# Kernel tuning notes

Measured on AMD Instinct MI355X. Metric: run time of the kernel, lower is better.

The kernel has to match this reference:

```python
import jax, jax.numpy as jnp
import numpy as np

NUM_LOW, NUM_HIGH, DIM = 8192, 1024, 2048
EPS = 1e-10


def sparsemax(z):
    # z: [..., K]; Martins & Astudillo sparsemax along last axis.
    K = z.shape[-1]
    z_sorted = jnp.flip(jnp.sort(z, axis=-1), axis=-1)          # descending
    z_cum = jnp.cumsum(z_sorted, axis=-1)
    k = jnp.arange(1, K + 1, dtype=z.dtype)
    support = (1.0 + k * z_sorted) > z_cum                       # bool [..., K]
    k_sup = jnp.sum(support, axis=-1, keepdims=True)             # int [..., 1]
    tau = (jnp.take_along_axis(z_cum, k_sup - 1, axis=-1) - 1.0) / k_sup.astype(z.dtype)
    return jnp.maximum(z - tau, 0.0)


def normalize_rows(x, eps=EPS):
    return x / (jnp.sum(x, axis=1, keepdims=True) + eps)


def setup_inputs() -> dict:
    key = jax.random.key(0)
    k1, k2, k3, k4 = jax.random.split(key, 4)

    def xavier(k, shape):
        bound = float(np.sqrt(6.0 / (shape[0] + shape[1])))
        return jax.random.uniform(k, shape, jnp.float32, -bound, bound)

    return {
        "low_w": xavier(k1, (NUM_LOW, DIM)),    # low Concepts parameter
        "high_w": xavier(k2, (NUM_HIGH, DIM)),  # high Concepts parameter
        "Wq": xavier(k3, (DIM, DIM)),           # q_linear.weight (keep_head_dim, n_head=1)
        "Wk": xavier(k4, (DIM, DIM)),           # k_linear.weight
        "norm_low_concepts": 1,
        "norm_high_concepts": 1,
    }


def reference(low_w, high_w, Wq, Wk, norm_low_concepts, norm_high_concepts):
    # Concepts modules: return (possibly normalized) concepts + cosine similarity.
    low_normed = low_w / jnp.linalg.norm(low_w, axis=1, keepdims=True)
    low_concepts = low_normed if norm_low_concepts else low_w
    low_cos = low_normed @ low_normed.T                          # [NL, NL]

    high_normed = high_w / jnp.linalg.norm(high_w, axis=1, keepdims=True)
    high_concepts = high_normed if norm_high_concepts else high_w
    high_cos = high_normed @ high_normed.T                       # [NH, NH]

    # detach_low_concepts=True -> queries do not receive gradients
    low_q = jax.lax.stop_gradient(low_concepts)

    # ModifiedMultiHeadAttention (n_head=1, keep_head_dim -> d_head=DIM; eval mode,
    # so smooth_max is identity and sparsemax is deterministic).
    q = low_q @ Wq.T                                             # [NL, D]
    k = high_concepts @ Wk.T                                     # [NH, D]
    scale = 1.0 / jnp.sqrt(jnp.asarray(DIM, q.dtype))
    attn = sparsemax((q @ k.T) * scale)                          # [NL, NH]
    high_related_low = attn @ high_concepts                      # [NL, D]

    # output_high_concepts_type == "high_plus_low": add back aggregated low concepts
    aggregated_low = normalize_rows(attn.T) @ low_q              # [NH, D]
    output_high_concepts = high_related_low + attn @ aggregated_low  # [NL, D]

    return (low_concepts, low_cos, output_high_concepts, high_cos, attn)
```

## Files before the change

kernel.cpp:

```cpp
#include <hip/hip_runtime.h>
#include <hip/hip_bf16.h>
#include <stdint.h>

#define NL   8192
#define NHI  1024
#define DIMV 2048

typedef __attribute__((ext_vector_type(8))) short short8;
typedef __attribute__((ext_vector_type(4))) float f32x4;

__device__ __forceinline__ unsigned short f2bf(float x){
  unsigned u = __float_as_uint(x);
  u += 0x7FFFu + ((u >> 16) & 1u);
  return (unsigned short)(u >> 16);
}
__device__ __forceinline__ float bf2f(unsigned short b){
  return __uint_as_float(((unsigned)b) << 16);
}
__device__ __forceinline__ unsigned pack2bf(float a, float b){
  return (unsigned)f2bf(a) | ((unsigned)f2bf(b) << 16);
}

__device__ __forceinline__ void gload16(const void* g, void* l){
  __builtin_amdgcn_global_load_lds(
      (const __attribute__((address_space(1))) unsigned int*)g,
      (__attribute__((address_space(3))) unsigned int*)l, 16, 0, 0);
}

template<int WRITE_F32>
__global__ __launch_bounds__(256)
void rownorm_kernel(const float* __restrict__ W, float* __restrict__ outF32,
                    unsigned short* __restrict__ outBf){
  int row = blockIdx.x;
  const float* r = W + (size_t)row * DIMV;
  int base = threadIdx.x * 8;
  float4 x0 = *(const float4*)(r + base);
  float4 x1 = *(const float4*)(r + base + 4);
  float ss = x0.x*x0.x + x0.y*x0.y + x0.z*x0.z + x0.w*x0.w
           + x1.x*x1.x + x1.y*x1.y + x1.z*x1.z + x1.w*x1.w;
  #pragma unroll
  for(int s = 1; s < 64; s <<= 1) ss += __shfl_xor(ss, s, 64);
  __shared__ float red[4];
  if((threadIdx.x & 63) == 0) red[threadIdx.x >> 6] = ss;
  __syncthreads();
  float tot = red[0] + red[1] + red[2] + red[3];
  float inv = 1.0f / sqrtf(tot);
  float y0=x0.x*inv, y1=x0.y*inv, y2=x0.z*inv, y3=x0.w*inv;
  float y4=x1.x*inv, y5=x1.y*inv, y6=x1.z*inv, y7=x1.w*inv;
  if(WRITE_F32){
    float* o = outF32 + (size_t)row * DIMV + base;
    *(float4*)o       = make_float4(y0,y1,y2,y3);
    *(float4*)(o + 4) = make_float4(y4,y5,y6,y7);
  }
  uint4 u;
  u.x = pack2bf(y0,y1); u.y = pack2bf(y2,y3);
  u.z = pack2bf(y4,y5); u.w = pack2bf(y6,y7);
  *(uint4*)(outBf + (size_t)row * DIMV + base) = u;
}

__global__ __launch_bounds__(256)
void cast2_kernel(const float* __restrict__ a, const float* __restrict__ b,
                  unsigned short* __restrict__ oa, unsigned short* __restrict__ ob){
  int id = blockIdx.x;
  const float* in; unsigned short* out;
  if(id < 2048){ in = a; out = oa; } else { in = b; out = ob; id -= 2048; }
  size_t i = ((size_t)id * 256 + threadIdx.x) * 8;
  float4 x0 = *(const float4*)(in + i);
  float4 x1 = *(const float4*)(in + i + 4);
  uint4 u;
  u.x = pack2bf(x0.x,x0.y); u.y = pack2bf(x0.z,x0.w);
  u.z = pack2bf(x1.x,x1.y); u.w = pack2bf(x1.z,x1.w);
  *(uint4*)(out + i) = u;
}

template<int OUT_BF16, int MIRROR>
__global__ __launch_bounds__(256, 2)
void gemm_bt_kernel(const unsigned short* __restrict__ A,
                    const unsigned short* __restrict__ Bt,
                    float* __restrict__ Cf, unsigned short* __restrict__ Cb,
                    int M, int N, int K, float scale){
  __shared__ __align__(16) char smem[32768];
  unsigned short* sA = (unsigned short*)smem;
  unsigned short* sB = sA + 128 * 64;

  int tid = threadIdx.x, lane = tid & 63, wid = tid >> 6;
  int mBase, nBase;
  if(MIRROR){
    int nwg = gridDim.x;
    int id = blockIdx.x;
    int cpx = nwg >> 3;
    id = (id & 7) * cpx + (id >> 3);
    int bi = 0;
    while(((bi+1)*64 - (((bi+1)*bi) >> 1)) <= id) bi++;
    int off = bi*64 - ((bi*(bi-1)) >> 1);
    int bj = bi + (id - off);
    mBase = bi * 128; nBase = bj * 128;
  } else {
    int gx = gridDim.x, gy = gridDim.y;
    int nwg = gx * gy;
    int id = blockIdx.y * gx + blockIdx.x;
    if((nwg & 7) == 0){ int cpx = nwg >> 3; id = (id & 7) * cpx + (id >> 3); }
    mBase = (id / gx) * 128; nBase = (id % gx) * 128;
  }

  int chRow = lane >> 3;
  int chCol = (lane & 7) * 8;
  int wm = wid >> 1, wn = wid & 1;

  f32x4 acc[4][4];
  #pragma unroll
  for(int i=0;i<4;i++)
    #pragma unroll
    for(int j=0;j<4;j++) acc[i][j] = (f32x4){0.f,0.f,0.f,0.f};

  int kChunk = K / (int)gridDim.z;
  int kStart = kChunk * (int)blockIdx.z;
  if(!OUT_BF16) Cf += (size_t)blockIdx.z * M * N;

  for(int k0 = kStart; k0 < kStart + kChunk; k0 += 64){
    #pragma unroll
    for(int i = 0; i < 4; i++){
      int ch = wid * 4 + i;
      int arow = ch * 8 + chRow;
      gload16(A  + (size_t)(mBase + arow) * K + k0 + chCol, &sA[ch * 512]);
      gload16(Bt + (size_t)(nBase + arow) * K + k0 + chCol, &sB[ch * 512]);
    }
    __syncthreads();
    #pragma unroll
    for(int kk = 0; kk < 64; kk += 32){
      short8 a[4], b[4];
      int krd = kk + (lane >> 4) * 8;
      #pragma unroll
      for(int i = 0; i < 4; i++){
        int row = wm * 64 + i * 16 + (lane & 15);
        a[i] = *reinterpret_cast<const short8*>(&sA[row * 64 + krd]);
        int col = wn * 64 + i * 16 + (lane & 15);
        b[i] = *reinterpret_cast<const short8*>(&sB[col * 64 + krd]);
      }
      #pragma unroll
      for(int i = 0; i < 4; i++)
        #pragma unroll
        for(int j = 0; j < 4; j++)
          acc[i][j] = __builtin_amdgcn_mfma_f32_16x16x32_bf16(a[i], b[j], acc[i][j], 0, 0, 0);
    }
    __syncthreads();
  }

  #pragma unroll
  for(int i = 0; i < 4; i++){
    #pragma unroll
    for(int j = 0; j < 4; j++){
      int row = mBase + wm * 64 + i * 16 + (lane >> 4) * 4;
      int col = nBase + wn * 64 + j * 16 + (lane & 15);
      #pragma unroll
      for(int r = 0; r < 4; r++){
        float v = acc[i][j][r] * scale;
        size_t off = (size_t)(row + r) * N + col;
        if(OUT_BF16) Cb[off] = f2bf(v);
        else         Cf[off] = v;
      }
    }
  }

  if(MIRROR && mBase != nBase){
    float* tf = (float*)smem;
    #pragma unroll
    for(int rq = 0; rq < 4; rq++){
      int qm = rq >> 1, qn = rq & 1;
      __syncthreads();
      if(wm == qm && wn == qn){
        #pragma unroll
        for(int i = 0; i < 4; i++)
          #pragma unroll
          for(int j = 0; j < 4; j++){
            int rl = i * 16 + (lane >> 4) * 4;
            int cl = j * 16 + (lane & 15);
            #pragma unroll
            for(int r = 0; r < 4; r++)
              tf[(rl + r) * 65 + cl] = acc[i][j][r] * scale;
          }
      }
      __syncthreads();
      int mr = tid >> 2, seg = tid & 3;
      size_t obase = (size_t)(nBase + qn * 64 + mr) * N + mBase + qm * 64 + seg * 16;
      #pragma unroll
      for(int k4 = 0; k4 < 4; k4++){
        float4 v;
        v.x = tf[(seg * 16 + k4 * 4 + 0) * 65 + mr];
        v.y = tf[(seg * 16 + k4 * 4 + 1) * 65 + mr];
        v.z = tf[(seg * 16 + k4 * 4 + 2) * 65 + mr];
        v.w = tf[(seg * 16 + k4 * 4 + 3) * 65 + mr];
        *(float4*)(Cf + obase + k4 * 4) = v;
      }
    }
  }
}

__global__ __launch_bounds__(256)
void combine_bf16_kernel(const float* __restrict__ p, unsigned short* __restrict__ out,
                         size_t stride){
  size_t i = ((size_t)blockIdx.x * 256 + threadIdx.x) * 8;
  float4 a0 = *(const float4*)(p + i);
  float4 a1 = *(const float4*)(p + i + 4);
  float4 b0 = *(const float4*)(p + stride + i);
  float4 b1 = *(const float4*)(p + stride + i + 4);
  uint4 u;
  u.x = pack2bf(a0.x+b0.x, a0.y+b0.y); u.y = pack2bf(a0.z+b0.z, a0.w+b0.w);
  u.z = pack2bf(a1.x+b1.x, a1.y+b1.y); u.w = pack2bf(a1.z+b1.z, a1.w+b1.w);
  *(uint4*)(out + i) = u;
}
__global__ __launch_bounds__(256)
void combine_f32_kernel(const float* __restrict__ p, float* __restrict__ out,
                        size_t stride){
  size_t i = ((size_t)blockIdx.x * 256 + threadIdx.x) * 8;
  float4 a0 = *(const float4*)(p + i);
  float4 a1 = *(const float4*)(p + i + 4);
  float4 b0 = *(const float4*)(p + stride + i);
  float4 b1 = *(const float4*)(p + stride + i + 4);
  *(float4*)(out + i)     = make_float4(a0.x+b0.x, a0.y+b0.y, a0.z+b0.z, a0.w+b0.w);
  *(float4*)(out + i + 4) = make_float4(a1.x+b1.x, a1.y+b1.y, a1.z+b1.z, a1.w+b1.w);
}

__global__ __launch_bounds__(256)
void sparsemax_kernel(float* __restrict__ S, unsigned short* __restrict__ attnBf){
  int wid = threadIdx.x >> 6, lane = threadIdx.x & 63;
  int row = blockIdx.x * 4 + wid;
  float* z = S + (size_t)row * NHI;
  float v[16];
  #pragma unroll
  for(int j = 0; j < 16; j++) v[j] = z[j * 64 + lane];
  float mx = v[0];
  #pragma unroll
  for(int j = 1; j < 16; j++) mx = fmaxf(mx, v[j]);
  #pragma unroll
  for(int s = 1; s < 64; s <<= 1) mx = fmaxf(mx, __shfl_xor(mx, s, 64));
  float lo = mx - 1.0f, hi = mx;
  for(int it = 0; it < 40; it++){
    float mid = 0.5f * (lo + hi);
    float sum = 0.f;
    #pragma unroll
    for(int j = 0; j < 16; j++) sum += fmaxf(v[j] - mid, 0.f);
    #pragma unroll
    for(int s = 1; s < 64; s <<= 1) sum += __shfl_xor(sum, s, 64);
    if(sum >= 1.0f) lo = mid; else hi = mid;
  }
  float cnt = 0.f, ssum = 0.f;
  #pragma unroll
  for(int j = 0; j < 16; j++){
    if(v[j] > lo){ cnt += 1.f; ssum += v[j]; }
  }
  #pragma unroll
  for(int s = 1; s < 64; s <<= 1){
    cnt  += __shfl_xor(cnt,  s, 64);
    ssum += __shfl_xor(ssum, s, 64);
  }
  float tau = (ssum - 1.0f) / cnt;
  #pragma unroll
  for(int j = 0; j < 16; j++){
    float a = fmaxf(v[j] - tau, 0.f);
    z[j * 64 + lane] = a;
    attnBf[(size_t)row * NHI + j * 64 + lane] = f2bf(a);
  }
}

__global__ __launch_bounds__(256)
void colsum_part_kernel(const float* __restrict__ attn, float* __restrict__ part){
  int chunk = blockIdx.x;
  int t = threadIdx.x;
  const float* p = attn + (size_t)chunk * 32 * NHI;
  float a0=0,a1=0,a2=0,a3=0;
  for(int r = 0; r < 32; r++){
    a0 += p[(size_t)r*NHI + t];
    a1 += p[(size_t)r*NHI + t + 256];
    a2 += p[(size_t)r*NHI + t + 512];
    a3 += p[(size_t)r*NHI + t + 768];
  }
  float* q = part + (size_t)chunk * NHI;
  q[t]=a0; q[t+256]=a1; q[t+512]=a2; q[t+768]=a3;
}
__global__ __launch_bounds__(256)
void colsum_final_kernel(const float* __restrict__ part, float* __restrict__ colsum){
  int c = blockIdx.x * 256 + threadIdx.x;
  float s = 0.f;
  for(int i = 0; i < 256; i++) s += part[(size_t)i * NHI + c];
  colsum[c] = s;
}

__global__ __launch_bounds__(256)
void transpose3_kernel(const unsigned short* __restrict__ attnB, unsigned short* __restrict__ attnT,
                       const unsigned short* __restrict__ lowN,  unsigned short* __restrict__ lowNT,
                       const unsigned short* __restrict__ highN, unsigned short* __restrict__ highNT){
  __shared__ unsigned short tile[64][65];
  int id = blockIdx.x;
  const unsigned short* in; unsigned short* out; int R, C, tx, ty;
  if(id < 2048){        in = attnB; out = attnT;  R = NL;  C = NHI;  tx = id & 15; ty = id >> 4; }
  else if(id < 6144){ id -= 2048;
                        in = lowN;  out = lowNT;  R = NL;  C = DIMV; tx = id & 31; ty = id >> 5; }
  else {              id -= 6144;
                        in = highN; out = highNT; R = NHI; C = DIMV; tx = id & 31; ty = id >> 5; }
  int c0 = tx * 64, r0 = ty * 64;
  int t = threadIdx.x;
  int ci = t & 63, r4 = t >> 6;
  #pragma unroll
  for(int k = 0; k < 16; k++){
    int r = k * 4 + r4;
    tile[r][ci] = in[(size_t)(r0 + r) * C + c0 + ci];
  }
  __syncthreads();
  #pragma unroll
  for(int k = 0; k < 16; k++){
    int cc = k * 4 + r4;
    out[(size_t)(c0 + cc) * R + r0 + ci] = tile[ci][cc];
  }
}

__global__ __launch_bounds__(256)
void mt_kernel(const unsigned short* __restrict__ highNT, const float* __restrict__ aggP,
               const float* __restrict__ colsum, unsigned short* __restrict__ Mt){
  int idx = blockIdx.x * 256 + threadIdx.x;
  int h = idx & 1023;
  float s = aggP[idx] + aggP[idx + 2097152] + aggP[idx + 4194304] + aggP[idx + 6291456];
  float val = bf2f(highNT[idx]) + s / (colsum[h] + 1e-10f);
  Mt[idx] = f2bf(val);
}

extern "C" void kernel_launch(void* const* d_in, const int* in_sizes, int n_in,
                              void* d_out, int out_size, void* d_ws, size_t ws_size,
                              hipStream_t stream){
  const float* low_w  = (const float*)d_in[0];
  const float* high_w = (const float*)d_in[1];
  const float* Wq     = (const float*)d_in[2];
  const float* Wk     = (const float*)d_in[3];
  float* out = (float*)d_out;

  char* ws = (char*)d_ws;
  unsigned short* lowN  = (unsigned short*)(ws);
  float*          aggP  = (float*)(ws);
  unsigned short* highN = (unsigned short*)(ws + 33554432);
  unsigned short* WqB   = (unsigned short*)(ws + 37748736);
  unsigned short* WkB   = (unsigned short*)(ws + 46137344);
  unsigned short* attnB = (unsigned short*)(ws + 37748736);
  unsigned short* qB    = (unsigned short*)(ws + 54525952);
  unsigned short* lowNT = qB;
  unsigned short* kB    = (unsigned short*)(ws + 88080384);
  float*          part  = (float*)(ws + 88080384);
  float*          colsum= (float*)(ws + 88080384 + 1048576);
  unsigned short* attnT = (unsigned short*)(ws + 92274688);
  float*          kPart = (float*)(ws + 92274688);
  unsigned short* Mt    = (unsigned short*)(ws + 109051904);
  unsigned short* highNT= (unsigned short*)(ws + 113246208);
  float*          hcPart= (float*)(ws + 109051904);

  float* out_lowc    = out;
  float* out_lowcos  = out + 16777216;
  float* out_high    = out + 83886080;
  float* out_highcos = out + 100663296;
  float* out_attn    = out + 101711872;

  const float scl = 1.0f / sqrtf((float)DIMV);

  rownorm_kernel<1><<<NL,  256, 0, stream>>>(low_w,  out_lowc, lowN);
  rownorm_kernel<0><<<NHI, 256, 0, stream>>>(high_w, nullptr,  highN);
  cast2_kernel<<<4096, 256, 0, stream>>>(Wq, Wk, WqB, WkB);
  gemm_bt_kernel<0,1><<<2080, 256, 0, stream>>>(lowN, lowN, out_lowcos, nullptr,
                                                NL, NL, DIMV, 1.0f);
  gemm_bt_kernel<0,0><<<dim3(8,8,2), 256, 0, stream>>>(highN, highN, hcPart, nullptr,
                                                       NHI, NHI, DIMV, 1.0f);
  combine_f32_kernel<<<512, 256, 0, stream>>>(hcPart, out_highcos, 1048576);
  gemm_bt_kernel<1,0><<<dim3(16,64), 256, 0, stream>>>(lowN, WqB, nullptr, qB,
                                                       NL, DIMV, DIMV, 1.0f);
  gemm_bt_kernel<0,0><<<dim3(16,8,2), 256, 0, stream>>>(highN, WkB, kPart, nullptr,
                                                        NHI, DIMV, DIMV, 1.0f);
  combine_bf16_kernel<<<1024, 256, 0, stream>>>(kPart, kB, 2097152);
  gemm_bt_kernel<0,0><<<dim3(8,64), 256, 0, stream>>>(qB, kB, out_attn, nullptr,
                                                      NL, NHI, DIMV, scl);
  sparsemax_kernel<<<NL/4, 256, 0, stream>>>(out_attn, attnB);
  colsum_part_kernel<<<256, 256, 0, stream>>>(out_attn, part);
  colsum_final_kernel<<<4, 256, 0, stream>>>(part, colsum);
  transpose3_kernel<<<6656, 256, 0, stream>>>(attnB, attnT, lowN, lowNT, highN, highNT);
  gemm_bt_kernel<0,0><<<dim3(8,16,4), 256, 0, stream>>>(lowNT, attnT, aggP, nullptr,
                                                        DIMV, NHI, NL, 1.0f);
  mt_kernel<<<8192, 256, 0, stream>>>(highNT, aggP, colsum, Mt);
  gemm_bt_kernel<0,0><<<dim3(16,64), 256, 0, stream>>>(attnB, Mt, out_high, nullptr,
                                                       NL, DIMV, NHI, 1.0f);
}
```

Before: 642.0 us.

## Fuse prep and combine kernels, make mirror transpose store per-wave without block syncs

Merges the two row-normalization launches and the weight cast into one prep kernel, and merges the two split-K combine kernels into one launch by reordering the Wk GEMM ahead of them. The mirrored lower-triangle write of the low cosine GEMM now transposes through a private LDS slice per wave instead of four block-wide passes with barriers, so each wave writes its own 64x64 quadrant in column strips. This removes launch overhead and __syncthreads stalls in the epilogue, at the cost of slightly larger LDS use per block, which could affect occupancy.

Result: slower. 657.5 us (+2.4%).

```diff
diff --git a/kernel.cpp b/kernel.cpp
--- a/kernel.cpp
+++ b/kernel.cpp
@@ -27,50 +27,53 @@
       (__attribute__((address_space(3))) unsigned int*)l, 16, 0, 0);
 }
 
-template<int WRITE_F32>
-__global__ __launch_bounds__(256)
-void rownorm_kernel(const float* __restrict__ W, float* __restrict__ outF32,
-                    unsigned short* __restrict__ outBf){
-  int row = blockIdx.x;
-  const float* r = W + (size_t)row * DIMV;
-  int base = threadIdx.x * 8;
-  float4 x0 = *(const float4*)(r + base);
-  float4 x1 = *(const float4*)(r + base + 4);
-  float ss = x0.x*x0.x + x0.y*x0.y + x0.z*x0.z + x0.w*x0.w
-           + x1.x*x1.x + x1.y*x1.y + x1.z*x1.z + x1.w*x1.w;
-  #pragma unroll
-  for(int s = 1; s < 64; s <<= 1) ss += __shfl_xor(ss, s, 64);
-  __shared__ float red[4];
-  if((threadIdx.x & 63) == 0) red[threadIdx.x >> 6] = ss;
-  __syncthreads();
-  float tot = red[0] + red[1] + red[2] + red[3];
-  float inv = 1.0f / sqrtf(tot);
-  float y0=x0.x*inv, y1=x0.y*inv, y2=x0.z*inv, y3=x0.w*inv;
-  float y4=x1.x*inv, y5=x1.y*inv, y6=x1.z*inv, y7=x1.w*inv;
-  if(WRITE_F32){
-    float* o = outF32 + (size_t)row * DIMV + base;
-    *(float4*)o       = make_float4(y0,y1,y2,y3);
-    *(float4*)(o + 4) = make_float4(y4,y5,y6,y7);
-  }
-  uint4 u;
-  u.x = pack2bf(y0,y1); u.y = pack2bf(y2,y3);
-  u.z = pack2bf(y4,y5); u.w = pack2bf(y6,y7);
-  *(uint4*)(outBf + (size_t)row * DIMV + base) = u;
-}
-
-__global__ __launch_bounds__(256)
-void cast2_kernel(const float* __restrict__ a, const float* __restrict__ b,
-                  unsigned short* __restrict__ oa, unsigned short* __restrict__ ob){
+__global__ __launch_bounds__(256)
+void prep_kernel(const float* __restrict__ low_w, const float* __restrict__ high_w,
+                 const float* __restrict__ Wq, const float* __restrict__ Wk,
+                 float* __restrict__ out_lowc, unsigned short* __restrict__ lowN,
+                 unsigned short* __restrict__ highN,
+                 unsigned short* __restrict__ WqB, unsigned short* __restrict__ WkB){
   int id = blockIdx.x;
-  const float* in; unsigned short* out;
-  if(id < 2048){ in = a; out = oa; } else { in = b; out = ob; id -= 2048; }
-  size_t i = ((size_t)id * 256 + threadIdx.x) * 8;
-  float4 x0 = *(const float4*)(in + i);
-  float4 x1 = *(const float4*)(in + i + 4);
-  uint4 u;
-  u.x = pack2bf(x0.x,x0.y); u.y = pack2bf(x0.z,x0.w);
-  u.z = pack2bf(x1.x,x1.y); u.w = pack2bf(x1.z,x1.w);
-  *(uint4*)(out + i) = u;
+  if(id < 9216){
+    const float* W; float* oF; unsigned short* oB; int row;
+    if(id < 8192){ W = low_w; oF = out_lowc; oB = lowN; row = id; }
+    else         { W = high_w; oF = nullptr; oB = highN; row = id - 8192; }
+    const float* r = W + (size_t)row * DIMV;
+    int base = threadIdx.x * 8;
+    float4 x0 = *(const float4*)(r + base);
+    float4 x1 = *(const float4*)(r + base + 4);
+    float ss = x0.x*x0.x + x0.y*x0.y + x0.z*x0.z + x0.w*x0.w
+             + x1.x*x1.x + x1.y*x1.y + x1.z*x1.z + x1.w*x1.w;
+    #pragma unroll
+    for(int s = 1; s < 64; s <<= 1) ss += __shfl_xor(ss, s, 64);
+    __shared__ float red[4];
+    if((threadIdx.x & 63) == 0) red[threadIdx.x >> 6] = ss;
+    __syncthreads();
+    float tot = red[0] + red[1] + red[2] + red[3];
+    float inv = 1.0f / sqrtf(tot);
+    float y0=x0.x*inv, y1=x0.y*inv, y2=x0.z*inv, y3=x0.w*inv;
+    float y4=x1.x*inv, y5=x1.y*inv, y6=x1.z*inv, y7=x1.w*inv;
+    if(oF){
+      float* o = oF + (size_t)row * DIMV + base;
+      *(float4*)o       = make_float4(y0,y1,y2,y3);
+      *(float4*)(o + 4) = make_float4(y4,y5,y6,y7);
+    }
+    uint4 u;
+    u.x = pack2bf(y0,y1); u.y = pack2bf(y2,y3);
+    u.z = pack2bf(y4,y5); u.w = pack2bf(y6,y7);
+    *(uint4*)(oB + (size_t)row * DIMV + base) = u;
+  } else {
+    id -= 9216;
+    const float* in; unsigned short* outp;
+    if(id < 2048){ in = Wq; outp = WqB; } else { in = Wk; outp = WkB; id -= 2048; }
+    size_t i = ((size_t)id * 256 + threadIdx.x) * 8;
+    float4 x0 = *(const float4*)(in + i);
+    float4 x1 = *(const float4*)(in + i + 4);
+    uint4 u;
+    u.x = pack2bf(x0.x,x0.y); u.y = pack2bf(x0.z,x0.w);
+    u.z = pack2bf(x1.x,x1.y); u.w = pack2bf(x1.z,x1.w);
+    *(uint4*)(outp + i) = u;
+  }
 }
 
 template<int OUT_BF16, int MIRROR>
@@ -79,7 +82,7 @@
                     const unsigned short* __restrict__ Bt,
                     float* __restrict__ Cf, unsigned short* __restrict__ Cb,
                     int M, int N, int K, float scale){
-  __shared__ __align__(16) char smem[32768];
+  __shared__ __align__(16) char smem[33792];
   unsigned short* sA = (unsigned short*)smem;
   unsigned short* sB = sA + 128 * 64;
 
@@ -163,62 +166,59 @@
   }
 
   if(MIRROR && mBase != nBase){
-    float* tf = (float*)smem;
-    #pragma unroll
-    for(int rq = 0; rq < 4; rq++){
-      int qm = rq >> 1, qn = rq & 1;
-      __syncthreads();
-      if(wm == qm && wn == qn){
+    float* T = (float*)(void*)(smem + wid * 8448);
+    int ln15 = lane & 15, lh = lane >> 4;
+    #pragma unroll
+    for(int hh = 0; hh < 2; hh++){
+      #pragma unroll
+      for(int ii = 0; ii < 2; ii++){
         #pragma unroll
-        for(int i = 0; i < 4; i++)
+        for(int j = 0; j < 4; j++)
           #pragma unroll
-          for(int j = 0; j < 4; j++){
-            int rl = i * 16 + (lane >> 4) * 4;
-            int cl = j * 16 + (lane & 15);
-            #pragma unroll
-            for(int r = 0; r < 4; r++)
-              tf[(rl + r) * 65 + cl] = acc[i][j][r] * scale;
-          }
+          for(int r = 0; r < 4; r++)
+            T[(j*16 + ln15)*33 + ii*16 + lh*4 + r] = acc[hh*2+ii][j][r] * scale;
       }
-      __syncthreads();
-      int mr = tid >> 2, seg = tid & 3;
-      size_t obase = (size_t)(nBase + qn * 64 + mr) * N + mBase + qm * 64 + seg * 16;
-      #pragma unroll
-      for(int k4 = 0; k4 < 4; k4++){
+      asm volatile("s_waitcnt lgkmcnt(0)" ::: "memory");
+      __builtin_amdgcn_sched_barrier(0);
+      size_t gb = (size_t)(nBase + wn*64 + lane) * N + (mBase + wm*64 + hh*32);
+      #pragma unroll
+      for(int k4 = 0; k4 < 8; k4++){
         float4 v;
-        v.x = tf[(seg * 16 + k4 * 4 + 0) * 65 + mr];
-        v.y = tf[(seg * 16 + k4 * 4 + 1) * 65 + mr];
-        v.z = tf[(seg * 16 + k4 * 4 + 2) * 65 + mr];
-        v.w = tf[(seg * 16 + k4 * 4 + 3) * 65 + mr];
-        *(float4*)(Cf + obase + k4 * 4) = v;
+        v.x = T[lane*33 + k4*4 + 0];
+        v.y = T[lane*33 + k4*4 + 1];
+        v.z = T[lane*33 + k4*4 + 2];
+        v.w = T[lane*33 + k4*4 + 3];
+        *(float4*)(Cf + gb + k4*4) = v;
       }
-    }
-  }
-}
-
-__global__ __launch_bounds__(256)
-void combine_bf16_kernel(const float* __restrict__ p, unsigned short* __restrict__ out,
-                         size_t stride){
-  size_t i = ((size_t)blockIdx.x * 256 + threadIdx.x) * 8;
-  float4 a0 = *(const float4*)(p + i);
-  float4 a1 = *(const float4*)(p + i + 4);
-  float4 b0 = *(const float4*)(p + stride + i);
-  float4 b1 = *(const float4*)(p + stride + i + 4);
-  uint4 u;
-  u.x = pack2bf(a0.x+b0.x, a0.y+b0.y); u.y = pack2bf(a0.z+b0.z, a0.w+b0.w);
-  u.z = pack2bf(a1.x+b1.x, a1.y+b1.y); u.w = pack2bf(a1.z+b1.z, a1.w+b1.w);
-  *(uint4*)(out + i) = u;
-}
-__global__ __launch_bounds__(256)
-void combine_f32_kernel(const float* __restrict__ p, float* __restrict__ out,
-                        size_t stride){
-  size_t i = ((size_t)blockIdx.x * 256 + threadIdx.x) * 8;
-  float4 a0 = *(const float4*)(p + i);
-  float4 a1 = *(const float4*)(p + i + 4);
-  float4 b0 = *(const float4*)(p + stride + i);
-  float4 b1 = *(const float4*)(p + stride + i + 4);
-  *(float4*)(out + i)     = make_float4(a0.x+b0.x, a0.y+b0.y, a0.z+b0.z, a0.w+b0.w);
-  *(float4*)(out + i + 4) = make_float4(a1.x+b1.x, a1.y+b1.y, a1.z+b1.z, a1.w+b1.w);
+      asm volatile("s_waitcnt lgkmcnt(0)" ::: "memory");
+      __builtin_amdgcn_sched_barrier(0);
+    }
+  }
+}
+
+__global__ __launch_bounds__(256)
+void combine2_kernel(const float* __restrict__ hcPart, float* __restrict__ out_highcos,
+                     const float* __restrict__ kPart, unsigned short* __restrict__ kB){
+  int id = blockIdx.x;
+  if(id < 512){
+    size_t i = ((size_t)id * 256 + threadIdx.x) * 8;
+    float4 a0 = *(const float4*)(hcPart + i);
+    float4 a1 = *(const float4*)(hcPart + i + 4);
+    float4 b0 = *(const float4*)(hcPart + 1048576 + i);
+    float4 b1 = *(const float4*)(hcPart + 1048576 + i + 4);
+    *(float4*)(out_highcos + i)     = make_float4(a0.x+b0.x, a0.y+b0.y, a0.z+b0.z, a0.w+b0.w);
+    *(float4*)(out_highcos + i + 4) = make_float4(a1.x+b1.x, a1.y+b1.y, a1.z+b1.z, a1.w+b1.w);
+  } else {
+    size_t i = ((size_t)(id - 512) * 256 + threadIdx.x) * 8;
+    float4 a0 = *(const float4*)(kPart + i);
+    float4 a1 = *(const float4*)(kPart + i + 4);
+    float4 b0 = *(const float4*)(kPart + 2097152 + i);
+    float4 b1 = *(const float4*)(kPart + 2097152 + i + 4);
+    uint4 u;
+    u.x = pack2bf(a0.x+b0.x, a0.y+b0.y); u.y = pack2bf(a0.z+b0.z, a0.w+b0.w);
+    u.z = pack2bf(a1.x+b1.x, a1.y+b1.y); u.w = pack2bf(a1.z+b1.z, a1.w+b1.w);
+    *(uint4*)(kB + i) = u;
+  }
 }
 
 __global__ __launch_bounds__(256)
@@ -359,19 +359,17 @@
 
   const float scl = 1.0f / sqrtf((float)DIMV);
 
-  rownorm_kernel<1><<<NL,  256, 0, stream>>>(low_w,  out_lowc, lowN);
-  rownorm_kernel<0><<<NHI, 256, 0, stream>>>(high_w, nullptr,  highN);
-  cast2_kernel<<<4096, 256, 0, stream>>>(Wq, Wk, WqB, WkB);
+  prep_kernel<<<13312, 256, 0, stream>>>(low_w, high_w, Wq, Wk,
+                                         out_lowc, lowN, highN, WqB, WkB);
   gemm_bt_kernel<0,1><<<2080, 256, 0, stream>>>(lowN, lowN, out_lowcos, nullptr,
                                                 NL, NL, DIMV, 1.0f);
   gemm_bt_kernel<0,0><<<dim3(8,8,2), 256, 0, stream>>>(highN, highN, hcPart, nullptr,
                                                        NHI, NHI, DIMV, 1.0f);
-  combine_f32_kernel<<<512, 256, 0, stream>>>(hcPart, out_highcos, 1048576);
+  gemm_bt_kernel<0,0><<<dim3(16,8,2), 256, 0, stream>>>(highN, WkB, kPart, nullptr,
+                                                        NHI, DIMV, DIMV, 1.0f);
+  combine2_kernel<<<1536, 256, 0, stream>>>(hcPart, out_highcos, kPart, kB);
   gemm_bt_kernel<1,0><<<dim3(16,64), 256, 0, stream>>>(lowN, WqB, nullptr, qB,
                                                        NL, DIMV, DIMV, 1.0f);
-  gemm_bt_kernel<0,0><<<dim3(16,8,2), 256, 0, stream>>>(highN, WkB, kPart, nullptr,
-                                                        NHI, DIMV, DIMV, 1.0f);
-  combine_bf16_kernel<<<1024, 256, 0, stream>>>(kPart, kB, 2097152);
   gemm_bt_kernel<0,0><<<dim3(8,64), 256, 0, stream>>>(qB, kB, out_attn, nullptr,
                                                       NL, NHI, DIMV, scl);
   sparsemax_kernel<<<NL/4, 256, 0, stream>>>(out_attn, attnB);
```
